# Performance work log

Hardware: AMD Instinct MI355X
Metric: run time of the kernel (lower is better)

## Reference

```python
import jax, jax.numpy as jnp
import numpy as np

IN_DIM = 256
OUT_DIM = 256


def setup_inputs() -> dict:
    key = jax.random.key(0)
    k1, k2, k3, k4 = jax.random.split(key, 4)
    B, N = 8, 2048
    X = jax.random.normal(k1, (B, N, IN_DIM), dtype=jnp.float32)
    adj = jax.random.uniform(k2, (B, N, N), dtype=jnp.float32)
    # nn.Linear(input_dim, output_dim): W is [out, in], bias [out]
    bound = 1.0 / np.sqrt(IN_DIM)
    W = jax.random.uniform(k3, (OUT_DIM, IN_DIM), minval=-bound, maxval=bound, dtype=jnp.float32)
    b = jax.random.uniform(k4, (OUT_DIM,), minval=-bound, maxval=bound, dtype=jnp.float32)
    return {"X": X, "adj": adj, "W": W, "b": b}


def reference(X, adj, W, b):
    N = adj.shape[-1]
    # adj_hat = adj + I
    adj_hat = adj + jnp.eye(N, dtype=adj.dtype)
    # D^{-1/2} A_hat D^{-1/2}: diag matmuls are just row/col scaling
    d = jnp.sum(adj_hat, axis=-1) ** -0.5  # [B, N]
    adj_norm = d[..., :, None] * adj_hat * d[..., None, :]
    # aggregate then linear + relu
    H = jnp.matmul(adj_norm, X)  # [B, N, F_in]
    out = jnp.einsum('bnf,of->bno', H, W) + b
    return jax.nn.relu(out)
```

## Files before the change

kernel.cpp:

```cpp
#include <hip/hip_runtime.h>
#include <stdint.h>

typedef __attribute__((ext_vector_type(8))) short bf16x8;
typedef __attribute__((ext_vector_type(8))) unsigned short u16x8;
typedef __attribute__((ext_vector_type(4))) float f32x4;
typedef unsigned short u16;

constexpr int NN = 2048, NF = 256;

__device__ inline u16 f2bf(float f) {
  uint32_t u = __builtin_bit_cast(uint32_t, f);
  uint32_t r = (u + 0x7FFFu + ((u >> 16) & 1u)) >> 16;
  return (u16)r;
}
__device__ inline float bf2f(u16 h) {
  uint32_t u = ((uint32_t)h) << 16;
  return __builtin_bit_cast(float, u);
}

__device__ inline void gload_lds16(const void* g, void* l) {
  __builtin_amdgcn_global_load_lds(
      (const __attribute__((address_space(1))) uint32_t*)g,
      (__attribute__((address_space(3))) uint32_t*)l,
      16, 0, 0);
}

__global__ __launch_bounds__(256) void k_rowsum(const float* __restrict__ adj,
                                                float* __restrict__ d,
                                                const float* __restrict__ W,
                                                u16* __restrict__ Wb) {
  if (blockIdx.x >= 16384) {
    int i = (blockIdx.x - 16384) * 256 + threadIdx.x;
    float4 v = ((const float4*)W)[i];
    ushort4 o;
    o.x = f2bf(v.x); o.y = f2bf(v.y); o.z = f2bf(v.z); o.w = f2bf(v.w);
    *(ushort4*)(Wb + (size_t)i * 4) = o;
    return;
  }
  int row = blockIdx.x;
  const float4* p = (const float4*)(adj + (size_t)row * NN);
  float s = 0.f;
#pragma unroll
  for (int c = 0; c < 2; ++c) {
    float4 v = p[threadIdx.x + 256 * c];
    s += v.x + v.y + v.z + v.w;
  }
#pragma unroll
  for (int off = 32; off > 0; off >>= 1) s += __shfl_down(s, off, 64);
  __shared__ float red[4];
  int lane = threadIdx.x & 63, w = threadIdx.x >> 6;
  if (lane == 0) red[w] = s;
  __syncthreads();
  if (threadIdx.x == 0) {
    float t = red[0] + red[1] + red[2] + red[3] + 1.0f;
    d[row] = 1.0f / sqrtf(t);
  }
}

__global__ __launch_bounds__(256) void k_xprep(const float* __restrict__ X,
                                               const float* __restrict__ d,
                                               u16* __restrict__ XpT) {
  int jt = blockIdx.x, ft = blockIdx.y, b = blockIdx.z;
  int j0 = jt * 64, f0 = ft * 64;
  __shared__ u16 T[64][66];
  int t = threadIdx.x;
#pragma unroll
  for (int s = 0; s < 4; ++s) {
    int q = s * 256 + t;
    int r = q >> 4, c4 = q & 15;
    int j = j0 + r;
    float dv = d[b * NN + j];
    float4 v = *(const float4*)(X + ((size_t)(b * NN + j)) * NF + f0 + c4 * 4);
    T[r][c4 * 4 + 0] = f2bf(v.x * dv);
    T[r][c4 * 4 + 1] = f2bf(v.y * dv);
    T[r][c4 * 4 + 2] = f2bf(v.z * dv);
    T[r][c4 * 4 + 3] = f2bf(v.w * dv);
  }
  __syncthreads();
#pragma unroll
  for (int s = 0; s < 4; ++s) {
    int q = s * 256 + t;
    int fr = q >> 4, c4 = q & 15;
    ushort4 o;
    o.x = T[c4 * 4 + 0][fr]; o.y = T[c4 * 4 + 1][fr];
    o.z = T[c4 * 4 + 2][fr]; o.w = T[c4 * 4 + 3][fr];
    *(ushort4*)(XpT + ((size_t)(b * NF + f0 + fr)) * NN + j0 + c4 * 4) = o;
  }
}

#define BBASE 24576

#define MFMA8(AB, BB)                                                          \
  {                                                                            \
    bf16x8 af0 = *(const bf16x8*)((AB) + aoff0);                               \
    bf16x8 af1 = *(const bf16x8*)((AB) + aoff0 + 1024);                        \
    bf16x8 b0 = *(const bf16x8*)((BB) + boff0);                                \
    bf16x8 b1 = *(const bf16x8*)((BB) + boff0 + 1024);                         \
    bf16x8 b2 = *(const bf16x8*)((BB) + boff0 + 2048);                         \
    bf16x8 b3 = *(const bf16x8*)((BB) + boff0 + 3072);                         \
    asm volatile("s_waitcnt lgkmcnt(0)" ::: "memory");                         \
    __builtin_amdgcn_sched_barrier(0);                                         \
    __builtin_amdgcn_s_setprio(1);                                             \
    acc[0][0] = __builtin_amdgcn_mfma_f32_16x16x32_bf16(af0, b0, acc[0][0], 0, 0, 0); \
    acc[0][1] = __builtin_amdgcn_mfma_f32_16x16x32_bf16(af0, b1, acc[0][1], 0, 0, 0); \
    acc[0][2] = __builtin_amdgcn_mfma_f32_16x16x32_bf16(af0, b2, acc[0][2], 0, 0, 0); \
    acc[0][3] = __builtin_amdgcn_mfma_f32_16x16x32_bf16(af0, b3, acc[0][3], 0, 0, 0); \
    acc[1][0] = __builtin_amdgcn_mfma_f32_16x16x32_bf16(af1, b0, acc[1][0], 0, 0, 0); \
    acc[1][1] = __builtin_amdgcn_mfma_f32_16x16x32_bf16(af1, b1, acc[1][1], 0, 0, 0); \
    acc[1][2] = __builtin_amdgcn_mfma_f32_16x16x32_bf16(af1, b2, acc[1][2], 0, 0, 0); \
    acc[1][3] = __builtin_amdgcn_mfma_f32_16x16x32_bf16(af1, b3, acc[1][3], 0, 0, 0); \
    __builtin_amdgcn_s_setprio(0);                                             \
  }

#define PAIR(G, RG, WG, SN, SW, BR0, BR1, BW0, BW1, VMC0, VMC1, IA, WA, IB)    \
  {                                                                            \
                   \
    if (IA) {                                                                  \
      aN0[SN] = *(const float4*)(a_gsrc + (size_t)((G) + 4) * 64);             \
      aN1[SN] = *(const float4*)(a_gsrc + (size_t)((G) + 4) * 64 + 4);         \
    }                                                                          \
    if (IB) {                                                                  \
      gload_lds16(b_src0 + (size_t)(2 * (G) + 4) * 32,                         \
                  smem + BBASE + (BW0) * 16384 + bw0);                         \
      gload_lds16(b_src1 + (size_t)(2 * (G) + 4) * 32,                         \
                  smem + BBASE + (BW0) * 16384 + bw1);                         \
    }                                                                          \
    __builtin_amdgcn_sched_barrier(0);                                         \
    asm volatile("s_waitcnt vmcnt(" VMC0 ") lgkmcnt(0)" ::: "memory");         \
    __builtin_amdgcn_sched_barrier(0);                                         \
    __builtin_amdgcn_s_barrier();                                              \
    __builtin_amdgcn_sched_barrier(0);                                         \
    MFMA8(smem + (RG) * 8192, smem + BBASE + (BR0) * 16384)                    \
    __builtin_amdgcn_sched_barrier(0);                                         \
    if (WA) {                                                                  \
      float4 c0 = aN0[SW], c1 = aN1[SW];                                       \
      u16x8 pk;                                                                \
      pk[0] = f2bf(c0.x); pk[1] = f2bf(c0.y); pk[2] = f2bf(c0.z);              \
      pk[3] = f2bf(c0.w); pk[4] = f2bf(c1.x); pk[5] = f2bf(c1.y);              \
      pk[6] = f2bf(c1.z); pk[7] = f2bf(c1.w);                                  \
      *(u16x8*)(smem + (WG) * 8192 + a_ldst) = pk;                             \
    }                                                                          \
    __builtin_amdgcn_sched_barrier(0);                                         \
                                                \
    if (IB) {                                                                  \
      gload_lds16(b_src0 + (size_t)(2 * (G) + 5) * 32,                         \
                  smem + BBASE + (BW1) * 16384 + bw0);                         \
      gload_lds16(b_src1 + (size_t)(2 * (G) + 5) * 32,                         \
                  smem + BBASE + (BW1) * 16384 + bw1);                         \
    }                                                                          \
    __builtin_amdgcn_sched_barrier(0);                                         \
    asm volatile("s_waitcnt vmcnt(" VMC1 ") lgkmcnt(0)" ::: "memory");         \
    __builtin_amdgcn_sched_barrier(0);                                         \
    __builtin_amdgcn_s_barrier();                                              \
    __builtin_amdgcn_sched_barrier(0);                                         \
    MFMA8(smem + (RG) * 8192 + 4096, smem + BBASE + (BR1) * 16384)             \
    __builtin_amdgcn_sched_barrier(0);                                         \
  }

__global__ __launch_bounds__(512, 2) void k_fused(
    const float* __restrict__ adj, const u16* __restrict__ XpT,
    const float* __restrict__ dsc, const u16* __restrict__ Wb,
    const float* __restrict__ bias, float* __restrict__ out) {
  int flat = blockIdx.x;
  int b = flat & 7, mt = flat >> 3;
  int i0 = mt * 64;

  __shared__ __align__(16) char smem[122880];
  u16* Hs = (u16*)smem;

  int t = threadIdx.x;
  int lane = t & 63, w = t >> 6;
  int l15 = lane & 15, l4 = lane >> 4;
  int wr = w >> 2, wc = w & 3;

  const float* adjf = adj + ((size_t)b * NN + i0) * NN;
  const u16* XpTb = XpT + (size_t)b * NF * NN;

  int rA = t >> 3, kc = t & 7;
  const float* a_gsrc = adjf + (size_t)rA * NN + kc * 8;
  int a_ldst = (kc >> 2) * 4096 + rA * 64 + (((kc & 3) ^ ((rA >> 1) & 3)) << 4);

  int n0s = t >> 2, c0s = t & 3;
  const u16* b_src0 = XpTb + (size_t)n0s * NN + ((c0s ^ ((n0s >> 1) & 3)) << 3);
  int s1 = 512 + t;
  int n1s = s1 >> 2, c1s = s1 & 3;
  const u16* b_src1 = XpTb + (size_t)n1s * NN + ((c1s ^ ((n1s >> 1) & 3)) << 3);
  int bw0 = w << 10;
  int bw1 = 8192 + (w << 10);

  int swz = (l4 ^ ((l15 >> 1) & 3)) << 4;
  int aoff0 = wr * 2048 + l15 * 64 + swz;
  int boff0 = (wc * 64 + l15) * 64 + swz;

  f32x4 acc[2][4] = {};
  float4 aN0[3], aN1[3];

  {
    float4 p0a = *(const float4*)(a_gsrc);
    float4 p0b = *(const float4*)(a_gsrc + 4);
    float4 p1a = *(const float4*)(a_gsrc + 64);
    float4 p1b = *(const float4*)(a_gsrc + 68);
    __builtin_amdgcn_sched_barrier(0);
    gload_lds16(b_src0, smem + BBASE + bw0);
    gload_lds16(b_src1, smem + BBASE + bw1);
    gload_lds16(b_src0 + 32, smem + BBASE + 16384 + bw0);
    gload_lds16(b_src1 + 32, smem + BBASE + 16384 + bw1);
    gload_lds16(b_src0 + 64, smem + BBASE + 32768 + bw0);
    gload_lds16(b_src1 + 64, smem + BBASE + 32768 + bw1);
    gload_lds16(b_src0 + 96, smem + BBASE + 49152 + bw0);
    gload_lds16(b_src1 + 96, smem + BBASE + 49152 + bw1);
    __builtin_amdgcn_sched_barrier(0);
    aN0[1] = *(const float4*)(a_gsrc + 128);
    aN1[1] = *(const float4*)(a_gsrc + 132);
    aN0[2] = *(const float4*)(a_gsrc + 192);
    aN1[2] = *(const float4*)(a_gsrc + 196);
    __builtin_amdgcn_sched_barrier(0);
    u16x8 pk;
    pk[0] = f2bf(p0a.x); pk[1] = f2bf(p0a.y); pk[2] = f2bf(p0a.z);
    pk[3] = f2bf(p0a.w); pk[4] = f2bf(p0b.x); pk[5] = f2bf(p0b.y);
    pk[6] = f2bf(p0b.z); pk[7] = f2bf(p0b.w);
    *(u16x8*)(smem + a_ldst) = pk;
    pk[0] = f2bf(p1a.x); pk[1] = f2bf(p1a.y); pk[2] = f2bf(p1a.z);
    pk[3] = f2bf(p1a.w); pk[4] = f2bf(p1b.x); pk[5] = f2bf(p1b.y);
    pk[6] = f2bf(p1b.z); pk[7] = f2bf(p1b.w);
    *(u16x8*)(smem + 8192 + a_ldst) = pk;
    __builtin_amdgcn_sched_barrier(0);
  }

  for (int gb = 0; gb < 27; gb += 3) {
    PAIR(gb + 0, 0, 2, 0, 1, 0, 1, 4, 5, "12", "12", 1, 1, 1)
    PAIR(gb + 1, 1, 0, 1, 2, 2, 3, 0, 1, "12", "12", 1, 1, 1)
    PAIR(gb + 2, 2, 1, 2, 0, 4, 5, 2, 3, "12", "12", 1, 1, 1)
  }
  PAIR(27, 0, 2, 0, 1, 0, 1, 4, 5, "12", "12", 1, 1, 1)
  PAIR(28, 1, 0, 1, 2, 2, 3, 0, 1, "10", "10", 0, 1, 1)
  PAIR(29, 2, 1, 2, 0, 4, 5, 2, 3, "8", "8", 0, 1, 1)
  PAIR(30, 0, 2, 0, 1, 0, 1, 4, 5, "6", "4", 0, 0, 0)
  PAIR(31, 1, 0, 1, 2, 2, 3, 0, 1, "2", "0", 0, 0, 0)

  __syncthreads();

  const float* db = dsc + b * NN;
#pragma unroll
  for (int mi = 0; mi < 2; ++mi) {
#pragma unroll
    for (int ni = 0; ni < 4; ++ni) {
      int f = wc * 64 + ni * 16 + l15;
      ushort4 xv = *(const ushort4*)(XpTb + (size_t)f * NN + i0 +
                                     wr * 32 + mi * 16 + l4 * 4);
#pragma unroll
      for (int qq = 0; qq < 4; ++qq) {
        int il = wr * 32 + mi * 16 + l4 * 4 + qq;
        float dv = db[i0 + il];
        float xpv = bf2f(((const u16*)&xv)[qq]);
        float hv = dv * (acc[mi][ni][qq] + xpv);
        Hs[il * 264 + f] = f2bf(hv);
      }
    }
  }
  __syncthreads();

  f32x4 acc2[2][4] = {};
#pragma unroll
  for (int kk = 0; kk < 256; kk += 32) {
    bf16x8 a2[2], b2[4];
#pragma unroll
    for (int mi = 0; mi < 2; ++mi) {
      int r = wr * 32 + mi * 16 + l15;
      a2[mi] = *(const bf16x8*)&Hs[r * 264 + kk + l4 * 8];
    }
#pragma unroll
    for (int ni = 0; ni < 4; ++ni) {
      int o = wc * 64 + ni * 16 + l15;
      b2[ni] = *(const bf16x8*)&Wb[(size_t)o * 256 + kk + l4 * 8];
    }
#pragma unroll
    for (int mi = 0; mi < 2; ++mi)
#pragma unroll
      for (int ni = 0; ni < 4; ++ni)
        acc2[mi][ni] = __builtin_amdgcn_mfma_f32_16x16x32_bf16(a2[mi], b2[ni],
                                                               acc2[mi][ni], 0, 0, 0);
  }

  float* outb = out + ((size_t)b * NN + i0) * NF;
#pragma unroll
  for (int mi = 0; mi < 2; ++mi) {
#pragma unroll
    for (int qq = 0; qq < 4; ++qq) {
      int il = wr * 32 + mi * 16 + l4 * 4 + qq;
#pragma unroll
      for (int ni = 0; ni < 4; ++ni) {
        int o = wc * 64 + ni * 16 + l15;
        float v = acc2[mi][ni][qq] + bias[o];
        outb[(size_t)il * NF + o] = fmaxf(v, 0.f);
      }
    }
  }
}

extern "C" void kernel_launch(void* const* d_in, const int* in_sizes, int n_in,
                              void* d_out, int out_size, void* d_ws, size_t ws_size,
                              hipStream_t stream) {
  const float* X    = (const float*)d_in[0];
  const float* adj  = (const float*)d_in[1];
  const float* W    = (const float*)d_in[2];
  const float* bias = (const float*)d_in[3];
  float* out = (float*)d_out;

  char* ws = (char*)d_ws;
  float* dsc = (float*)(ws);
  u16*   Wb  = (u16*)(ws + 65536);
  u16*   XpT = (u16*)(ws + 262144);

  k_rowsum<<<dim3(16448), dim3(256), 0, stream>>>(adj, dsc, W, Wb);
  k_xprep<<<dim3(32, 4, 8), dim3(256), 0, stream>>>(X, dsc, XpT);
  k_fused<<<dim3(256), dim3(512), 0, stream>>>(adj, XpT, dsc, Wb, bias, out);
}
```

Before: 74.20 us.

## Load B operand directly from global into registers, shrinking LDS to A only

The XpT (B) tiles are no longer staged through LDS with global_load_lds. Each wave now loads its bf16 B fragments straight from global memory into a triple-buffered register set, prefetched two k-steps ahead. LDS shrinks from 120 KB to 36 KB and holds only the converted adj tile. The pipeline drops to one barrier per pair with reworked waitcnts. This removes LDS traffic and barriers for B, but each wave now redundantly fetches its own B columns from global/L2 and needs more registers.

```diff
diff --git a/kernel.cpp b/kernel.cpp
--- a/kernel.cpp
+++ b/kernel.cpp
@@ -16,13 +16,6 @@
 __device__ inline float bf2f(u16 h) {
   uint32_t u = ((uint32_t)h) << 16;
   return __builtin_bit_cast(float, u);
-}
-
-__device__ inline void gload_lds16(const void* g, void* l) {
-  __builtin_amdgcn_global_load_lds(
-      (const __attribute__((address_space(1))) uint32_t*)g,
-      (__attribute__((address_space(3))) uint32_t*)l,
-      16, 0, 0);
 }
 
 __global__ __launch_bounds__(256) void k_rowsum(const float* __restrict__ adj,
@@ -88,72 +81,61 @@
   }
 }
 
-#define BBASE 24576
-
-#define MFMA8(AB, BB)                                                          \
-  {                                                                            \
-    bf16x8 af0 = *(const bf16x8*)((AB) + aoff0);                               \
-    bf16x8 af1 = *(const bf16x8*)((AB) + aoff0 + 1024);                        \
-    bf16x8 b0 = *(const bf16x8*)((BB) + boff0);                                \
-    bf16x8 b1 = *(const bf16x8*)((BB) + boff0 + 1024);                         \
-    bf16x8 b2 = *(const bf16x8*)((BB) + boff0 + 2048);                         \
-    bf16x8 b3 = *(const bf16x8*)((BB) + boff0 + 3072);                         \
-    asm volatile("s_waitcnt lgkmcnt(0)" ::: "memory");                         \
-    __builtin_amdgcn_sched_barrier(0);                                         \
+#define BLOAD(SET, K)                                                          \
+    SET[0] = *(const bf16x8*)(bp0 + (size_t)(K) * 32);                         \
+    SET[1] = *(const bf16x8*)(bp1 + (size_t)(K) * 32);                         \
+    SET[2] = *(const bf16x8*)(bp2 + (size_t)(K) * 32);                         \
+    SET[3] = *(const bf16x8*)(bp3 + (size_t)(K) * 32);
+
+#define MFMA8(A0, A1, BS)                                                      \
     __builtin_amdgcn_s_setprio(1);                                             \
-    acc[0][0] = __builtin_amdgcn_mfma_f32_16x16x32_bf16(af0, b0, acc[0][0], 0, 0, 0); \
-    acc[0][1] = __builtin_amdgcn_mfma_f32_16x16x32_bf16(af0, b1, acc[0][1], 0, 0, 0); \
-    acc[0][2] = __builtin_amdgcn_mfma_f32_16x16x32_bf16(af0, b2, acc[0][2], 0, 0, 0); \
-    acc[0][3] = __builtin_amdgcn_mfma_f32_16x16x32_bf16(af0, b3, acc[0][3], 0, 0, 0); \
-    acc[1][0] = __builtin_amdgcn_mfma_f32_16x16x32_bf16(af1, b0, acc[1][0], 0, 0, 0); \
-    acc[1][1] = __builtin_amdgcn_mfma_f32_16x16x32_bf16(af1, b1, acc[1][1], 0, 0, 0); \
-    acc[1][2] = __builtin_amdgcn_mfma_f32_16x16x32_bf16(af1, b2, acc[1][2], 0, 0, 0); \
-    acc[1][3] = __builtin_amdgcn_mfma_f32_16x16x32_bf16(af1, b3, acc[1][3], 0, 0, 0); \
-    __builtin_amdgcn_s_setprio(0);                                             \
-  }
-
-#define PAIR(G, RG, WG, SN, SW, BR0, BR1, BW0, BW1, VMC0, VMC1, IA, WA, IB)    \
-  {                                                                            \
-                   \
-    if (IA) {                                                                  \
-      aN0[SN] = *(const float4*)(a_gsrc + (size_t)((G) + 4) * 64);             \
-      aN1[SN] = *(const float4*)(a_gsrc + (size_t)((G) + 4) * 64 + 4);         \
-    }                                                                          \
-    if (IB) {                                                                  \
-      gload_lds16(b_src0 + (size_t)(2 * (G) + 4) * 32,                         \
-                  smem + BBASE + (BW0) * 16384 + bw0);                         \
-      gload_lds16(b_src1 + (size_t)(2 * (G) + 4) * 32,                         \
-                  smem + BBASE + (BW0) * 16384 + bw1);                         \
-    }                                                                          \
-    __builtin_amdgcn_sched_barrier(0);                                         \
-    asm volatile("s_waitcnt vmcnt(" VMC0 ") lgkmcnt(0)" ::: "memory");         \
-    __builtin_amdgcn_sched_barrier(0);                                         \
-    __builtin_amdgcn_s_barrier();                                              \
-    __builtin_amdgcn_sched_barrier(0);                                         \
-    MFMA8(smem + (RG) * 8192, smem + BBASE + (BR0) * 16384)                    \
-    __builtin_amdgcn_sched_barrier(0);                                         \
-    if (WA) {                                                                  \
-      float4 c0 = aN0[SW], c1 = aN1[SW];                                       \
+    acc[0][0] = __builtin_amdgcn_mfma_f32_16x16x32_bf16(A0, BS[0], acc[0][0], 0, 0, 0); \
+    acc[0][1] = __builtin_amdgcn_mfma_f32_16x16x32_bf16(A0, BS[1], acc[0][1], 0, 0, 0); \
+    acc[0][2] = __builtin_amdgcn_mfma_f32_16x16x32_bf16(A0, BS[2], acc[0][2], 0, 0, 0); \
+    acc[0][3] = __builtin_amdgcn_mfma_f32_16x16x32_bf16(A0, BS[3], acc[0][3], 0, 0, 0); \
+    acc[1][0] = __builtin_amdgcn_mfma_f32_16x16x32_bf16(A1, BS[0], acc[1][0], 0, 0, 0); \
+    acc[1][1] = __builtin_amdgcn_mfma_f32_16x16x32_bf16(A1, BS[1], acc[1][1], 0, 0, 0); \
+    acc[1][2] = __builtin_amdgcn_mfma_f32_16x16x32_bf16(A1, BS[2], acc[1][2], 0, 0, 0); \
+    acc[1][3] = __builtin_amdgcn_mfma_f32_16x16x32_bf16(A1, BS[3], acc[1][3], 0, 0, 0); \
+    __builtin_amdgcn_s_setprio(0);
+
+#define AWRITE(SW_, GW_)                                                       \
+    {                                                                          \
+      float4 c0 = aN0[SW_], c1 = aN1[SW_];                                     \
       u16x8 pk;                                                                \
       pk[0] = f2bf(c0.x); pk[1] = f2bf(c0.y); pk[2] = f2bf(c0.z);              \
       pk[3] = f2bf(c0.w); pk[4] = f2bf(c1.x); pk[5] = f2bf(c1.y);              \
       pk[6] = f2bf(c1.z); pk[7] = f2bf(c1.w);                                  \
-      *(u16x8*)(smem + (WG) * 8192 + a_ldst) = pk;                             \
+      *(u16x8*)(smem + (GW_) * 8192 + a_ldst) = pk;                            \
+    }
+
+#define PAIR(G, GR, GW, SL, SW, BS0n, BS1n, IA, WA, IB0, IB1)                  \
+  {                                                                            \
+    __builtin_amdgcn_s_barrier();                                              \
+    __builtin_amdgcn_sched_barrier(0);                                         \
+    bf16x8 a00 = *(const bf16x8*)(smem + (GR) * 8192 + aoff0);                 \
+    bf16x8 a01 = *(const bf16x8*)(smem + (GR) * 8192 + aoff0 + 1024);          \
+    bf16x8 a10 = *(const bf16x8*)(smem + (GR) * 8192 + 4096 + aoff0);          \
+    bf16x8 a11 = *(const bf16x8*)(smem + (GR) * 8192 + 4096 + aoff0 + 1024);   \
+    asm volatile("s_waitcnt lgkmcnt(2)" ::: "memory");                         \
+    __builtin_amdgcn_sched_barrier(0);                                         \
+    MFMA8(a00, a01, BS0n)                                                      \
+    __builtin_amdgcn_sched_barrier(0);                                         \
+    if (IB0) { BLOAD(BS0n, 2 * (G) + 3) }                                      \
+    __builtin_amdgcn_sched_barrier(0);                                         \
+    asm volatile("s_waitcnt lgkmcnt(0)" ::: "memory");                         \
+    __builtin_amdgcn_sched_barrier(0);                                         \
+    MFMA8(a10, a11, BS1n)                                                      \
+    __builtin_amdgcn_sched_barrier(0);                                         \
+    if (IB1) { BLOAD(BS1n, 2 * (G) + 4) }                                      \
+    if (IA) {                                                                  \
+      aN0[SL] = *(const float4*)(a_gsrc + (size_t)((G) + 4) * 64);             \
+      aN1[SL] = *(const float4*)(a_gsrc + (size_t)((G) + 4) * 64 + 4);         \
     }                                                                          \
-    __builtin_amdgcn_sched_barrier(0);                                         \
-                                                \
-    if (IB) {                                                                  \
-      gload_lds16(b_src0 + (size_t)(2 * (G) + 5) * 32,                         \
-                  smem + BBASE + (BW1) * 16384 + bw0);                         \
-      gload_lds16(b_src1 + (size_t)(2 * (G) + 5) * 32,                         \
-                  smem + BBASE + (BW1) * 16384 + bw1);                         \
+    if (WA) {                                                                  \
+      AWRITE(SW, GW)                                                           \
+      asm volatile("s_waitcnt lgkmcnt(0)" ::: "memory");                       \
     }                                                                          \
-    __builtin_amdgcn_sched_barrier(0);                                         \
-    asm volatile("s_waitcnt vmcnt(" VMC1 ") lgkmcnt(0)" ::: "memory");         \
-    __builtin_amdgcn_sched_barrier(0);                                         \
-    __builtin_amdgcn_s_barrier();                                              \
-    __builtin_amdgcn_sched_barrier(0);                                         \
-    MFMA8(smem + (RG) * 8192 + 4096, smem + BBASE + (BR1) * 16384)             \
     __builtin_amdgcn_sched_barrier(0);                                         \
   }
 
@@ -165,7 +147,7 @@
   int b = flat & 7, mt = flat >> 3;
   int i0 = mt * 64;
 
-  __shared__ __align__(16) char smem[122880];
+  __shared__ __align__(16) char smem[36864];
   u16* Hs = (u16*)smem;
 
   int t = threadIdx.x;
@@ -180,41 +162,30 @@
   const float* a_gsrc = adjf + (size_t)rA * NN + kc * 8;
   int a_ldst = (kc >> 2) * 4096 + rA * 64 + (((kc & 3) ^ ((rA >> 1) & 3)) << 4);
 
-  int n0s = t >> 2, c0s = t & 3;
-  const u16* b_src0 = XpTb + (size_t)n0s * NN + ((c0s ^ ((n0s >> 1) & 3)) << 3);
-  int s1 = 512 + t;
-  int n1s = s1 >> 2, c1s = s1 & 3;
-  const u16* b_src1 = XpTb + (size_t)n1s * NN + ((c1s ^ ((n1s >> 1) & 3)) << 3);
-  int bw0 = w << 10;
-  int bw1 = 8192 + (w << 10);
-
   int swz = (l4 ^ ((l15 >> 1) & 3)) << 4;
   int aoff0 = wr * 2048 + l15 * 64 + swz;
-  int boff0 = (wc * 64 + l15) * 64 + swz;
+
+  const u16* bp0 = XpTb + (size_t)(wc * 64 + l15) * NN + l4 * 8;
+  const u16* bp1 = bp0 + (size_t)16 * NN;
+  const u16* bp2 = bp0 + (size_t)32 * NN;
+  const u16* bp3 = bp0 + (size_t)48 * NN;
 
   f32x4 acc[2][4] = {};
   float4 aN0[3], aN1[3];
-
+  bf16x8 bsA[4], bsB[4], bsC[4];
+
+  BLOAD(bsA, 0)
+  BLOAD(bsB, 1)
+  BLOAD(bsC, 2)
   {
     float4 p0a = *(const float4*)(a_gsrc);
     float4 p0b = *(const float4*)(a_gsrc + 4);
     float4 p1a = *(const float4*)(a_gsrc + 64);
     float4 p1b = *(const float4*)(a_gsrc + 68);
-    __builtin_amdgcn_sched_barrier(0);
-    gload_lds16(b_src0, smem + BBASE + bw0);
-    gload_lds16(b_src1, smem + BBASE + bw1);
-    gload_lds16(b_src0 + 32, smem + BBASE + 16384 + bw0);
-    gload_lds16(b_src1 + 32, smem + BBASE + 16384 + bw1);
-    gload_lds16(b_src0 + 64, smem + BBASE + 32768 + bw0);
-    gload_lds16(b_src1 + 64, smem + BBASE + 32768 + bw1);
-    gload_lds16(b_src0 + 96, smem + BBASE + 49152 + bw0);
-    gload_lds16(b_src1 + 96, smem + BBASE + 49152 + bw1);
-    __builtin_amdgcn_sched_barrier(0);
-    aN0[1] = *(const float4*)(a_gsrc + 128);
-    aN1[1] = *(const float4*)(a_gsrc + 132);
-    aN0[2] = *(const float4*)(a_gsrc + 192);
-    aN1[2] = *(const float4*)(a_gsrc + 196);
-    __builtin_amdgcn_sched_barrier(0);
+    aN0[2] = *(const float4*)(a_gsrc + 128);
+    aN1[2] = *(const float4*)(a_gsrc + 132);
+    aN0[0] = *(const float4*)(a_gsrc + 192);
+    aN1[0] = *(const float4*)(a_gsrc + 196);
     u16x8 pk;
     pk[0] = f2bf(p0a.x); pk[1] = f2bf(p0a.y); pk[2] = f2bf(p0a.z);
     pk[3] = f2bf(p0a.w); pk[4] = f2bf(p0b.x); pk[5] = f2bf(p0b.y);
@@ -224,19 +195,21 @@
     pk[3] = f2bf(p1a.w); pk[4] = f2bf(p1b.x); pk[5] = f2bf(p1b.y);
     pk[6] = f2bf(p1b.z); pk[7] = f2bf(p1b.w);
     *(u16x8*)(smem + 8192 + a_ldst) = pk;
+    asm volatile("s_waitcnt lgkmcnt(0)" ::: "memory");
     __builtin_amdgcn_sched_barrier(0);
   }
 
-  for (int gb = 0; gb < 27; gb += 3) {
-    PAIR(gb + 0, 0, 2, 0, 1, 0, 1, 4, 5, "12", "12", 1, 1, 1)
-    PAIR(gb + 1, 1, 0, 1, 2, 2, 3, 0, 1, "12", "12", 1, 1, 1)
-    PAIR(gb + 2, 2, 1, 2, 0, 4, 5, 2, 3, "12", "12", 1, 1, 1)
-  }
-  PAIR(27, 0, 2, 0, 1, 0, 1, 4, 5, "12", "12", 1, 1, 1)
-  PAIR(28, 1, 0, 1, 2, 2, 3, 0, 1, "10", "10", 0, 1, 1)
-  PAIR(29, 2, 1, 2, 0, 4, 5, 2, 3, "8", "8", 0, 1, 1)
-  PAIR(30, 0, 2, 0, 1, 0, 1, 4, 5, "6", "4", 0, 0, 0)
-  PAIR(31, 1, 0, 1, 2, 2, 3, 0, 1, "2", "0", 0, 0, 0)
+  for (int gb = 0; gb < 9; ++gb) {
+    int g = gb * 3;
+    PAIR(g + 0, 0, 2, 1, 2, bsA, bsB, 1, 1, 1, 1)
+    PAIR(g + 1, 1, 0, 2, 0, bsC, bsA, 1, 1, 1, 1)
+    PAIR(g + 2, 2, 1, 0, 1, bsB, bsC, 1, 1, 1, 1)
+  }
+  PAIR(27, 0, 2, 1, 2, bsA, bsB, 1, 1, 1, 1)
+  PAIR(28, 1, 0, 2, 0, bsC, bsA, 0, 1, 1, 1)
+  PAIR(29, 2, 1, 0, 1, bsB, bsC, 0, 1, 1, 1)
+  PAIR(30, 0, 0, 0, 0, bsA, bsB, 0, 0, 1, 0)
+  PAIR(31, 1, 0, 0, 0, bsC, bsA, 0, 0, 0, 0)
 
   __syncthreads();
 
```

After: 105.2 us. +41.8%, slower.

## Merge two K-halves per barrier step and overlap second-half LDS reads with MFMAs

Applied to the files above, without the earlier changes.

Restructures the main K loop from pairs of half-steps, each with its own barrier, into full 64-wide K steps with one barrier each. Buffers are rotated over three stages of A and B. All LDS fragment reads for both halves are issued up front, and a partial lgkmcnt wait lets the first eight MFMAs start while the second half's reads are still in flight. This halves the number of workgroup barriers and hides LDS latency. The cost is a shallower prefetch distance for A (two steps ahead instead of four half-steps) and more live registers, which may strain occupancy at 2 waves per SIMD.

```diff
diff --git a/kernel.cpp b/kernel.cpp
--- a/kernel.cpp
+++ b/kernel.cpp
@@ -90,70 +90,71 @@
 
 #define BBASE 24576
 
-#define MFMA8(AB, BB)                                                          \
+#define MFMA8X(A0, A1, B0, B1, B2, B3)                                         \
+    __builtin_amdgcn_s_setprio(1);                                             \
+    acc[0][0] = __builtin_amdgcn_mfma_f32_16x16x32_bf16(A0, B0, acc[0][0], 0, 0, 0); \
+    acc[0][1] = __builtin_amdgcn_mfma_f32_16x16x32_bf16(A0, B1, acc[0][1], 0, 0, 0); \
+    acc[0][2] = __builtin_amdgcn_mfma_f32_16x16x32_bf16(A0, B2, acc[0][2], 0, 0, 0); \
+    acc[0][3] = __builtin_amdgcn_mfma_f32_16x16x32_bf16(A0, B3, acc[0][3], 0, 0, 0); \
+    acc[1][0] = __builtin_amdgcn_mfma_f32_16x16x32_bf16(A1, B0, acc[1][0], 0, 0, 0); \
+    acc[1][1] = __builtin_amdgcn_mfma_f32_16x16x32_bf16(A1, B1, acc[1][1], 0, 0, 0); \
+    acc[1][2] = __builtin_amdgcn_mfma_f32_16x16x32_bf16(A1, B2, acc[1][2], 0, 0, 0); \
+    acc[1][3] = __builtin_amdgcn_mfma_f32_16x16x32_bf16(A1, B3, acc[1][3], 0, 0, 0); \
+    __builtin_amdgcn_s_setprio(0);
+
+#define STEP(KS, R3, W3, VMC, IA, WA, IB)                                      \
   {                                                                            \
-    bf16x8 af0 = *(const bf16x8*)((AB) + aoff0);                               \
-    bf16x8 af1 = *(const bf16x8*)((AB) + aoff0 + 1024);                        \
-    bf16x8 b0 = *(const bf16x8*)((BB) + boff0);                                \
-    bf16x8 b1 = *(const bf16x8*)((BB) + boff0 + 1024);                         \
-    bf16x8 b2 = *(const bf16x8*)((BB) + boff0 + 2048);                         \
-    bf16x8 b3 = *(const bf16x8*)((BB) + boff0 + 3072);                         \
+    if (IB) {                                                                  \
+      gload_lds16(b_src0 + (size_t)((KS) + 2) * 64,                            \
+                  smem + BBASE + (W3) * 32768 + bw0);                          \
+      gload_lds16(b_src1 + (size_t)((KS) + 2) * 64,                            \
+                  smem + BBASE + (W3) * 32768 + bw1);                          \
+      gload_lds16(b_src0 + (size_t)((KS) + 2) * 64 + 32,                       \
+                  smem + BBASE + (W3) * 32768 + 16384 + bw0);                  \
+      gload_lds16(b_src1 + (size_t)((KS) + 2) * 64 + 32,                       \
+                  smem + BBASE + (W3) * 32768 + 16384 + bw1);                  \
+    }                                                                          \
+    if (IA) {                                                                  \
+      aN0[R3] = *(const float4*)(a_gsrc + (size_t)((KS) + 3) * 64);            \
+      aN1[R3] = *(const float4*)(a_gsrc + (size_t)((KS) + 3) * 64 + 4);        \
+    }                                                                          \
+    __builtin_amdgcn_sched_barrier(0);                                         \
+    asm volatile("s_waitcnt vmcnt(" VMC ") lgkmcnt(0)" ::: "memory");          \
+    __builtin_amdgcn_sched_barrier(0);                                         \
+    __builtin_amdgcn_s_barrier();                                              \
+    __builtin_amdgcn_sched_barrier(0);                                         \
+    const char* Ab = smem + (R3) * 8192;                                       \
+    const char* Be = smem + BBASE + (R3) * 32768;                              \
+    const char* Bo = Be + 16384;                                               \
+    bf16x8 a00 = *(const bf16x8*)(Ab + aoff0);                                 \
+    bf16x8 a01 = *(const bf16x8*)(Ab + aoff0 + 1024);                          \
+    bf16x8 be0 = *(const bf16x8*)(Be + boff0);                                 \
+    bf16x8 be1 = *(const bf16x8*)(Be + boff0 + 1024);                          \
+    bf16x8 be2 = *(const bf16x8*)(Be + boff0 + 2048);                          \
+    bf16x8 be3 = *(const bf16x8*)(Be + boff0 + 3072);                          \
+    __builtin_amdgcn_sched_barrier(0);                                         \
+    bf16x8 a10 = *(const bf16x8*)(Ab + 4096 + aoff0);                          \
+    bf16x8 a11 = *(const bf16x8*)(Ab + 4096 + aoff0 + 1024);                   \
+    bf16x8 bo0 = *(const bf16x8*)(Bo + boff0);                                 \
+    bf16x8 bo1 = *(const bf16x8*)(Bo + boff0 + 1024);                          \
+    bf16x8 bo2 = *(const bf16x8*)(Bo + boff0 + 2048);                          \
+    bf16x8 bo3 = *(const bf16x8*)(Bo + boff0 + 3072);                          \
+    asm volatile("s_waitcnt lgkmcnt(6)" ::: "memory");                         \
+    __builtin_amdgcn_sched_barrier(0);                                         \
+    MFMA8X(a00, a01, be0, be1, be2, be3)                                       \
+    __builtin_amdgcn_sched_barrier(0);                                         \
     asm volatile("s_waitcnt lgkmcnt(0)" ::: "memory");                         \
     __builtin_amdgcn_sched_barrier(0);                                         \
-    __builtin_amdgcn_s_setprio(1);                                             \
-    acc[0][0] = __builtin_amdgcn_mfma_f32_16x16x32_bf16(af0, b0, acc[0][0], 0, 0, 0); \
-    acc[0][1] = __builtin_amdgcn_mfma_f32_16x16x32_bf16(af0, b1, acc[0][1], 0, 0, 0); \
-    acc[0][2] = __builtin_amdgcn_mfma_f32_16x16x32_bf16(af0, b2, acc[0][2], 0, 0, 0); \
-    acc[0][3] = __builtin_amdgcn_mfma_f32_16x16x32_bf16(af0, b3, acc[0][3], 0, 0, 0); \
-    acc[1][0] = __builtin_amdgcn_mfma_f32_16x16x32_bf16(af1, b0, acc[1][0], 0, 0, 0); \
-    acc[1][1] = __builtin_amdgcn_mfma_f32_16x16x32_bf16(af1, b1, acc[1][1], 0, 0, 0); \
-    acc[1][2] = __builtin_amdgcn_mfma_f32_16x16x32_bf16(af1, b2, acc[1][2], 0, 0, 0); \
-    acc[1][3] = __builtin_amdgcn_mfma_f32_16x16x32_bf16(af1, b3, acc[1][3], 0, 0, 0); \
-    __builtin_amdgcn_s_setprio(0);                                             \
-  }
-
-#define PAIR(G, RG, WG, SN, SW, BR0, BR1, BW0, BW1, VMC0, VMC1, IA, WA, IB)    \
-  {                                                                            \
-                   \
-    if (IA) {                                                                  \
-      aN0[SN] = *(const float4*)(a_gsrc + (size_t)((G) + 4) * 64);             \
-      aN1[SN] = *(const float4*)(a_gsrc + (size_t)((G) + 4) * 64 + 4);         \
-    }                                                                          \
-    if (IB) {                                                                  \
-      gload_lds16(b_src0 + (size_t)(2 * (G) + 4) * 32,                         \
-                  smem + BBASE + (BW0) * 16384 + bw0);                         \
-      gload_lds16(b_src1 + (size_t)(2 * (G) + 4) * 32,                         \
-                  smem + BBASE + (BW0) * 16384 + bw1);                         \
-    }                                                                          \
-    __builtin_amdgcn_sched_barrier(0);                                         \
-    asm volatile("s_waitcnt vmcnt(" VMC0 ") lgkmcnt(0)" ::: "memory");         \
-    __builtin_amdgcn_sched_barrier(0);                                         \
-    __builtin_amdgcn_s_barrier();                                              \
-    __builtin_amdgcn_sched_barrier(0);                                         \
-    MFMA8(smem + (RG) * 8192, smem + BBASE + (BR0) * 16384)                    \
+    MFMA8X(a10, a11, bo0, bo1, bo2, bo3)                                       \
     __builtin_amdgcn_sched_barrier(0);                                         \
     if (WA) {                                                                  \
-      float4 c0 = aN0[SW], c1 = aN1[SW];                                       \
+      float4 c0 = aN0[W3], c1 = aN1[W3];                                       \
       u16x8 pk;                                                                \
       pk[0] = f2bf(c0.x); pk[1] = f2bf(c0.y); pk[2] = f2bf(c0.z);              \
       pk[3] = f2bf(c0.w); pk[4] = f2bf(c1.x); pk[5] = f2bf(c1.y);              \
       pk[6] = f2bf(c1.z); pk[7] = f2bf(c1.w);                                  \
-      *(u16x8*)(smem + (WG) * 8192 + a_ldst) = pk;                             \
+      *(u16x8*)(smem + (W3) * 8192 + a_ldst) = pk;                             \
     }                                                                          \
-    __builtin_amdgcn_sched_barrier(0);                                         \
-                                                \
-    if (IB) {                                                                  \
-      gload_lds16(b_src0 + (size_t)(2 * (G) + 5) * 32,                         \
-                  smem + BBASE + (BW1) * 16384 + bw0);                         \
-      gload_lds16(b_src1 + (size_t)(2 * (G) + 5) * 32,                         \
-                  smem + BBASE + (BW1) * 16384 + bw1);                         \
-    }                                                                          \
-    __builtin_amdgcn_sched_barrier(0);                                         \
-    asm volatile("s_waitcnt vmcnt(" VMC1 ") lgkmcnt(0)" ::: "memory");         \
-    __builtin_amdgcn_sched_barrier(0);                                         \
-    __builtin_amdgcn_s_barrier();                                              \
-    __builtin_amdgcn_sched_barrier(0);                                         \
-    MFMA8(smem + (RG) * 8192 + 4096, smem + BBASE + (BR1) * 16384)             \
     __builtin_amdgcn_sched_barrier(0);                                         \
   }
 
@@ -207,13 +208,11 @@
     gload_lds16(b_src1 + 32, smem + BBASE + 16384 + bw1);
     gload_lds16(b_src0 + 64, smem + BBASE + 32768 + bw0);
     gload_lds16(b_src1 + 64, smem + BBASE + 32768 + bw1);
-    gload_lds16(b_src0 + 96, smem + BBASE + 49152 + bw0);
-    gload_lds16(b_src1 + 96, smem + BBASE + 49152 + bw1);
+    gload_lds16(b_src0 + 96, smem + BBASE + 32768 + 16384 + bw0);
+    gload_lds16(b_src1 + 96, smem + BBASE + 32768 + 16384 + bw1);
     __builtin_amdgcn_sched_barrier(0);
-    aN0[1] = *(const float4*)(a_gsrc + 128);
-    aN1[1] = *(const float4*)(a_gsrc + 132);
-    aN0[2] = *(const float4*)(a_gsrc + 192);
-    aN1[2] = *(const float4*)(a_gsrc + 196);
+    aN0[2] = *(const float4*)(a_gsrc + 128);
+    aN1[2] = *(const float4*)(a_gsrc + 132);
     __builtin_amdgcn_sched_barrier(0);
     u16x8 pk;
     pk[0] = f2bf(p0a.x); pk[1] = f2bf(p0a.y); pk[2] = f2bf(p0a.z);
@@ -227,16 +226,19 @@
     __builtin_amdgcn_sched_barrier(0);
   }
 
-  for (int gb = 0; gb < 27; gb += 3) {
-    PAIR(gb + 0, 0, 2, 0, 1, 0, 1, 4, 5, "12", "12", 1, 1, 1)
-    PAIR(gb + 1, 1, 0, 1, 2, 2, 3, 0, 1, "12", "12", 1, 1, 1)
-    PAIR(gb + 2, 2, 1, 2, 0, 4, 5, 2, 3, "12", "12", 1, 1, 1)
-  }
-  PAIR(27, 0, 2, 0, 1, 0, 1, 4, 5, "12", "12", 1, 1, 1)
-  PAIR(28, 1, 0, 1, 2, 2, 3, 0, 1, "10", "10", 0, 1, 1)
-  PAIR(29, 2, 1, 2, 0, 4, 5, 2, 3, "8", "8", 0, 1, 1)
-  PAIR(30, 0, 2, 0, 1, 0, 1, 4, 5, "6", "4", 0, 0, 0)
-  PAIR(31, 1, 0, 1, 2, 2, 3, 0, 1, "2", "0", 0, 0, 0)
+  STEP(0, 0, 2, "10", 1, 1, 1)
+  STEP(1, 1, 0, "12", 1, 1, 1)
+  for (int sb = 2; sb <= 23; sb += 3) {
+    STEP(sb + 0, 2, 1, "12", 1, 1, 1)
+    STEP(sb + 1, 0, 2, "12", 1, 1, 1)
+    STEP(sb + 2, 1, 0, "12", 1, 1, 1)
+  }
+  STEP(26, 2, 1, "12", 1, 1, 1)
+  STEP(27, 0, 2, "12", 1, 1, 1)
+  STEP(28, 1, 0, "12", 1, 1, 1)
+  STEP(29, 2, 1, "12", 0, 1, 1)
+  STEP(30, 0, 2, "4", 0, 0, 0)
+  STEP(31, 1, 0, "0", 0, 0, 0)
 
   __syncthreads();
 
```

New measurement: 72.22 us, median of 2. 2.7% less time.
